# Optimization experiments

Measured on AMD Instinct MI355X. Metric: run time of the kernel, lower is better.

## Reference

```python
import jax, jax.numpy as jnp
from jax import lax
import numpy as np

B, T, D_IN, H, D_L1_IN = 128, 2048, 5, 128, 256


def _gru_layer(x, w_ih, w_hh, b_ih, b_hh, reverse):
    # x: [B,T,D]; w_ih: [3H,D]; w_hh: [3H,H]. PyTorch gate order: r, z, n.
    gx = jnp.einsum('btd,gd->btg', x, w_ih) + b_ih  # [B,T,3H] input projections, batched
    if reverse:
        gx = gx[:, ::-1]
    gx_t = jnp.swapaxes(gx, 0, 1)  # [T,B,3H]
    h0 = jnp.zeros((x.shape[0], H), x.dtype)

    def step(h, gxt):
        gh = h @ w_hh.T + b_hh  # [B,3H]
        r = jax.nn.sigmoid(gxt[:, :H] + gh[:, :H])
        z = jax.nn.sigmoid(gxt[:, H:2 * H] + gh[:, H:2 * H])
        n = jnp.tanh(gxt[:, 2 * H:] + r * gh[:, 2 * H:])
        h_new = (1.0 - z) * n + z * h
        return h_new, h_new

    _, ys = lax.scan(step, h0, gx_t)  # ys: [T,B,H]
    ys = jnp.swapaxes(ys, 0, 1)  # [B,T,H]
    if reverse:
        ys = ys[:, ::-1]
    return ys


def setup_inputs() -> dict:
    key = jax.random.key(0)
    ks = jax.random.split(key, 16)
    s0 = 1.0 / np.sqrt(H)

    def w(k, shape):
        return jax.random.uniform(k, shape, jnp.float32, -s0, s0)

    inp = {'seq': jax.random.normal(ks[0], (B, T, D_IN), jnp.float32)}
    # layer 0 forward / backward (input dim 5)
    inp['w_ih_l0f'] = w(ks[1], (3 * H, D_IN)); inp['w_hh_l0f'] = w(ks[2], (3 * H, H))
    inp['b_ih_l0f'] = w(ks[3], (3 * H,));      inp['b_hh_l0f'] = w(ks[4], (3 * H,))
    inp['w_ih_l0b'] = w(ks[5], (3 * H, D_IN)); inp['w_hh_l0b'] = w(ks[6], (3 * H, H))
    inp['b_ih_l0b'] = w(ks[7], (3 * H,));      inp['b_hh_l0b'] = w(ks[8], (3 * H,))
    # layer 1 forward / backward (input dim 256 = 2*H)
    inp['w_ih_l1f'] = w(ks[9], (3 * H, D_L1_IN));  inp['w_hh_l1f'] = w(ks[10], (3 * H, H))
    inp['b_ih_l1f'] = w(ks[11], (3 * H,));         inp['b_hh_l1f'] = w(ks[12], (3 * H,))
    inp['w_ih_l1b'] = w(ks[13], (3 * H, D_L1_IN)); inp['w_hh_l1b'] = w(ks[14], (3 * H, H))
    inp['b_ih_l1b'] = w(ks[15], (3 * H,));         inp['b_hh_l1b'] = w(ks[15], (3 * H,)) * 0.9
    # linear head
    kf = jax.random.split(ks[0], 2)
    inp['fc_w'] = w(kf[0], (1, 2 * H))
    inp['fc_b'] = w(kf[1], (1,))
    return inp


def reference(seq, w_ih_l0f, w_hh_l0f, b_ih_l0f, b_hh_l0f,
              w_ih_l0b, w_hh_l0b, b_ih_l0b, b_hh_l0b,
              w_ih_l1f, w_hh_l1f, b_ih_l1f, b_hh_l1f,
              w_ih_l1b, w_hh_l1b, b_ih_l1b, b_hh_l1b,
              fc_w, fc_b):
    # layer 0: bidirectional, concat directions
    y0f = _gru_layer(seq, w_ih_l0f, w_hh_l0f, b_ih_l0f, b_hh_l0f, reverse=False)
    y0b = _gru_layer(seq, w_ih_l0b, w_hh_l0b, b_ih_l0b, b_hh_l0b, reverse=True)
    y0 = jnp.concatenate([y0f, y0b], axis=-1)  # [B,T,256]
    # layer 1
    y1f = _gru_layer(y0, w_ih_l1f, w_hh_l1f, b_ih_l1f, b_hh_l1f, reverse=False)
    y1b = _gru_layer(y0, w_ih_l1b, w_hh_l1b, b_ih_l1b, b_hh_l1b, reverse=True)
    y1 = jnp.concatenate([y1f, y1b], axis=-1)  # [B,T,256]
    # head on last timestep
    return y1[:, -1, :] @ fc_w.T + fc_b  # [B,1]
```

## Files before the change

### kernel.cpp

```cpp
#include <hip/hip_runtime.h>
#include <hip/hip_fp16.h>
#include <cstdint>

#define B_   128
#define T_   2048
#define DIN  5
#define H_   128
#define G3   384
#define D1   256
#define CH   256
#define NCH  (T_ / CH)

typedef _Float16 half8 __attribute__((ext_vector_type(8)));
typedef float f32x4 __attribute__((ext_vector_type(4)));

__device__ __forceinline__ float sigmoid_f(float x) {
    return __builtin_amdgcn_rcpf(1.0f + __expf(-x));
}
__device__ __forceinline__ float tanh_f(float x) {
    return 1.0f - 2.0f * __builtin_amdgcn_rcpf(__expf(2.0f * x) + 1.0f);
}
__device__ __forceinline__ unsigned long long pack4h(const float* h) {
    union { __half2 h2[2]; unsigned long long u; } pk;
    pk.h2[0] = __floats2half2_rn(h[0], h[1]);
    pk.h2[1] = __floats2half2_rn(h[2], h[3]);
    return pk.u;
}
__device__ __forceinline__ f32x4 h4_to_f(unsigned long long u) {
    union { unsigned long long u; __half2 h2[2]; } p; p.u = u;
    const float2 a = __half22float2(p.h2[0]);
    const float2 b = __half22float2(p.h2[1]);
    f32x4 r; r[0] = a.x; r[1] = a.y; r[2] = b.x; r[3] = b.y; return r;
}
__device__ __forceinline__ void fast_barrier() {
    asm volatile("s_waitcnt lgkmcnt(0)\n\ts_barrier" ::: "memory");
}

__global__ __launch_bounds__(256, 1) void scan0_mfma3(
    const float* __restrict__ seq,
    const float* __restrict__ wihf, const float* __restrict__ whhf,
    const float* __restrict__ bihf, const float* __restrict__ bhhf,
    const float* __restrict__ wihb, const float* __restrict__ whhb,
    const float* __restrict__ bihb, const float* __restrict__ bhhb,
    __half* __restrict__ y0)
{
    const int tid = threadIdx.x;
    const int w  = tid >> 6;
    const int l  = tid & 63;
    const int lo = l & 15;
    const int g  = l >> 4;
    const int dir = blockIdx.x >> 3;
    const int bg  = blockIdx.x & 7;

    const float* w_ih = dir ? wihb : wihf;
    const float* w_hh = dir ? whhb : whhf;
    const float* b_ih = dir ? bihb : bihf;
    const float* b_hh = dir ? bhhb : bhhf;

    __shared__ __align__(16) char smem[2 * 16 * 512];

    half8 a_r[2][5], a_z[2][5], a_n[2][5], a_x[2];
#pragma unroll
    for (int i = 0; i < 2; ++i) {
        const int grow = (2 * w + i) * 16 + lo;
#pragma unroll
        for (int c = 0; c < 5; ++c) {
            half8 vr, vz, vn;
#pragma unroll
            for (int j = 0; j < 8; ++j) {
                const int k = c * 32 + g * 8 + j;
                float fr, fz, fn;
                if (k < 128) {
                    fr = w_hh[grow * H_ + k];
                    fz = w_hh[(128 + grow) * H_ + k];
                    fn = w_hh[(256 + grow) * H_ + k];
                } else if (k < 133) {
                    fr = w_ih[grow * DIN + (k - 128)];
                    fz = w_ih[(128 + grow) * DIN + (k - 128)];
                    fn = 0.f;
                } else if (k == 133) {
                    fr = b_ih[grow] + b_hh[grow];
                    fz = b_ih[128 + grow] + b_hh[128 + grow];
                    fn = b_hh[256 + grow];
                } else { fr = 0.f; fz = 0.f; fn = 0.f; }
                vr[j] = (_Float16)fr; vz[j] = (_Float16)fz; vn[j] = (_Float16)fn;
            }
            a_r[i][c] = vr; a_z[i][c] = vz; a_n[i][c] = vn;
        }
        half8 vx;
#pragma unroll
        for (int j = 0; j < 8; ++j) {
            const int k = 128 + g * 8 + j;
            float f = 0.f;
            if (k < 133)       f = w_ih[(256 + grow) * DIN + (k - 128)];
            else if (k == 133) f = b_ih[256 + grow];
            vx[j] = (_Float16)f;
        }
        a_x[i] = vx;
    }

#pragma unroll
    for (int q = 0; q < 4; ++q) {
        f32x4 z = {0.f, 0.f, 0.f, 0.f};
        *reinterpret_cast<f32x4*>(smem + tid * 64 + q * 16) = z;
    }
    __syncthreads();
    if (tid < 32) {
        const int row = tid & 15, bu = tid >> 4;
        *(_Float16*)(smem + bu * 8192 + row * 512 + (266 ^ ((row & 7) << 4))) =
            (_Float16)1.0f;
    }
    const bool stager = tid < 80;
    const int sb = tid / 5, sd = tid % 5;
    const size_t seqbase = (size_t)(bg * 16 + sb) * T_ * DIN + sd;
    float x_t1 = 0.f;
    if (stager) {
        const int tt0 = dir ? (T_ - 1) : 0;
        const float x0 = seq[seqbase + (size_t)tt0 * DIN];
        *(_Float16*)(smem + sb * 512 + ((256 + 2 * sd) ^ ((sb & 7) << 4))) =
            (_Float16)x0;
        const int tt1 = dir ? (T_ - 2) : 1;
        x_t1 = seq[seqbase + (size_t)tt1 * DIN];
    }
    __syncthreads();

    float h_old[2][4];
#pragma unroll
    for (int i = 0; i < 2; ++i)
#pragma unroll
        for (int q = 0; q < 4; ++q) h_old[i][q] = 0.f;

    for (int t = 0; t < T_; ++t) {
        char* cur = smem + (t & 1) * 8192;
        char* nxt = smem + ((t + 1) & 1) * 8192;

        if (stager)
            *(_Float16*)(nxt + sb * 512 + ((256 + 2 * sd) ^ ((sb & 7) << 4))) =
                (_Float16)x_t1;

        half8 bf[5];
#pragma unroll
        for (int c = 0; c < 5; ++c)
            bf[c] = *reinterpret_cast<const half8*>(
                cur + lo * 512 + ((c * 64 + g * 16) ^ ((lo & 7) << 4)));

        float x_t2 = 0.f;
        if (stager) {
            const int t2 = (t + 2 < T_) ? t + 2 : T_ - 1;
            const int tt2 = dir ? (T_ - 1 - t2) : t2;
            x_t2 = seq[seqbase + (size_t)tt2 * DIN];
        }

        f32x4 accr[2], accz[2], accn[2], accx[2];
#pragma unroll
        for (int i = 0; i < 2; ++i) {
            f32x4 zr = {0.f, 0.f, 0.f, 0.f};
            accr[i] = zr; accz[i] = zr; accn[i] = zr;
#pragma unroll
            for (int c = 0; c < 5; ++c) {
                accr[i] = __builtin_amdgcn_mfma_f32_16x16x32_f16(a_r[i][c], bf[c], accr[i], 0, 0, 0);
                accz[i] = __builtin_amdgcn_mfma_f32_16x16x32_f16(a_z[i][c], bf[c], accz[i], 0, 0, 0);
                accn[i] = __builtin_amdgcn_mfma_f32_16x16x32_f16(a_n[i][c], bf[c], accn[i], 0, 0, 0);
            }
            accx[i] = __builtin_amdgcn_mfma_f32_16x16x32_f16(a_x[i], bf[4], zr, 0, 0, 0);
        }

        const int tt = dir ? (T_ - 1 - t) : t;
#pragma unroll
        for (int i = 0; i < 2; ++i) {
            float hn[4];
#pragma unroll
            for (int q = 0; q < 4; ++q) {
                const float r = sigmoid_f(accr[i][q]);
                const float z = sigmoid_f(accz[i][q]);
                const float n = tanh_f(accx[i][q] + r * accn[i][q]);
                hn[q] = n + z * (h_old[i][q] - n);
                h_old[i][q] = hn[q];
            }
            const int j0 = (2 * w + i) * 16 + g * 4;
            const unsigned long long pu = pack4h(hn);
            *reinterpret_cast<unsigned long long*>(
                &y0[((size_t)(bg * 16 + lo) * T_ + tt) * D1 + dir * H_ + j0]) = pu;
            *reinterpret_cast<unsigned long long*>(
                nxt + lo * 512 + ((2 * j0) ^ ((lo & 7) << 4))) = pu;
        }
        x_t1 = x_t2;
        fast_barrier();
    }
}

__global__ __launch_bounds__(256, 2) void gemm1_f16(
    const __half* __restrict__ A,
    const float* __restrict__ W,
    const float* __restrict__ bias,
    __half* __restrict__ C,
    int c0)
{
    __shared__ __align__(16) _Float16 As[128][32];
    __shared__ __align__(16) _Float16 Bs[64][32];
    const int tid = threadIdx.x;
    const int wave = tid >> 6, l = tid & 63;
    const int wm = wave >> 1, wn = wave & 1;
    const int lo = l & 15, g = l >> 4;
    const int m0 = blockIdx.x * 128, n0 = blockIdx.y * 64;

    f32x4 acc[4][2];
#pragma unroll
    for (int mt = 0; mt < 4; ++mt)
#pragma unroll
        for (int nt = 0; nt < 2; ++nt) {
            f32x4 z = {0.f, 0.f, 0.f, 0.f};
            acc[mt][nt] = z;
        }

    for (int kc = 0; kc < 256; kc += 32) {
#pragma unroll
        for (int r2 = 0; r2 < 2; ++r2) {
            const int idx = tid + r2 * 256;
            const int row = idx >> 2, seg = idx & 3;
            const int m = m0 + row, bb = m >> 8, tlq = m & (CH - 1);
            const __half* src = A + ((size_t)bb * T_ + c0 + tlq) * D1 + kc + seg * 8;
            *reinterpret_cast<uint4*>(&As[row][seg * 8]) =
                *reinterpret_cast<const uint4*>(src);
        }
        {
            const int row = tid >> 2, seg = tid & 3;
            const float* srcw = W + (size_t)(n0 + row) * D1 + kc + seg * 8;
            const float4 u0 = *reinterpret_cast<const float4*>(srcw);
            const float4 u1 = *reinterpret_cast<const float4*>(srcw + 4);
            half8 hv;
            hv[0] = (_Float16)u0.x; hv[1] = (_Float16)u0.y;
            hv[2] = (_Float16)u0.z; hv[3] = (_Float16)u0.w;
            hv[4] = (_Float16)u1.x; hv[5] = (_Float16)u1.y;
            hv[6] = (_Float16)u1.z; hv[7] = (_Float16)u1.w;
            *reinterpret_cast<half8*>(&Bs[row][seg * 8]) = hv;
        }
        __syncthreads();
        half8 af[4], bfr[2];
#pragma unroll
        for (int mt = 0; mt < 4; ++mt)
            af[mt] = *reinterpret_cast<half8*>(&As[wm * 64 + mt * 16 + lo][g * 8]);
#pragma unroll
        for (int nt = 0; nt < 2; ++nt)
            bfr[nt] = *reinterpret_cast<half8*>(&Bs[wn * 32 + nt * 16 + lo][g * 8]);
#pragma unroll
        for (int mt = 0; mt < 4; ++mt)
#pragma unroll
            for (int nt = 0; nt < 2; ++nt)
                acc[mt][nt] = __builtin_amdgcn_mfma_f32_16x16x32_f16(
                    af[mt], bfr[nt], acc[mt][nt], 0, 0, 0);
        __syncthreads();
    }
#pragma unroll
    for (int nt = 0; nt < 2; ++nt) {
        const int n = n0 + wn * 32 + nt * 16 + lo;
        const float bv = bias[n];
#pragma unroll
        for (int mt = 0; mt < 4; ++mt) {
            const int mrow = m0 + wm * 64 + mt * 16 + g * 4;
#pragma unroll
            for (int q = 0; q < 4; ++q)
                C[(size_t)(mrow + q) * G3 + n] = __float2half(acc[mt][nt][q] + bv);
        }
    }
}

__global__ __launch_bounds__(256, 1) void scan1_mfma3(
    const __half* __restrict__ gxc,
    const float* __restrict__ whh, const float* __restrict__ bhh,
    float* __restrict__ h1, int c)
{
    const int tid = threadIdx.x;
    const int w = tid >> 6, l = tid & 63;
    const int lo = l & 15, g = l >> 4;
    const int grp = blockIdx.x;

    __shared__ __align__(16) char smem[2 * 16 * 256];

    half8 a_r[2][4], a_z[2][4], a_n[2][4];
    float br[2][4], bz[2][4], bn[2][4];
#pragma unroll
    for (int i = 0; i < 2; ++i) {
        const int grow = (2 * w + i) * 16 + lo;
#pragma unroll
        for (int cc = 0; cc < 4; ++cc) {
            half8 vr, vz, vn;
#pragma unroll
            for (int j = 0; j < 8; ++j) {
                const int k = cc * 32 + g * 8 + j;
                vr[j] = (_Float16)whh[grow * H_ + k];
                vz[j] = (_Float16)whh[(128 + grow) * H_ + k];
                vn[j] = (_Float16)whh[(256 + grow) * H_ + k];
            }
            a_r[i][cc] = vr; a_z[i][cc] = vz; a_n[i][cc] = vn;
        }
#pragma unroll
        for (int q = 0; q < 4; ++q) {
            const int gq = (2 * w + i) * 16 + g * 4 + q;
            br[i][q] = bhh[gq];
            bz[i][q] = bhh[128 + gq];
            bn[i][q] = bhh[256 + gq];
        }
    }

#pragma unroll
    for (int q = 0; q < 2; ++q) {
        f32x4 z = {0.f, 0.f, 0.f, 0.f};
        *reinterpret_cast<f32x4*>(smem + tid * 32 + q * 16) = z;
    }
    __syncthreads();

    float h_old[2][4];
    if (c == 0) {
#pragma unroll
        for (int i = 0; i < 2; ++i)
#pragma unroll
            for (int q = 0; q < 4; ++q) h_old[i][q] = 0.f;
    } else {
#pragma unroll
        for (int i = 0; i < 2; ++i) {
            const int j0 = (2 * w + i) * 16 + g * 4;
            const f32x4 hv = *reinterpret_cast<const f32x4*>(
                &h1[(grp * 16 + lo) * H_ + j0]);
            float hn[4];
#pragma unroll
            for (int q = 0; q < 4; ++q) { h_old[i][q] = hv[q]; hn[q] = hv[q]; }
            *reinterpret_cast<unsigned long long*>(
                smem + lo * 256 + ((2 * j0) ^ ((lo & 7) << 4))) = pack4h(hn);
        }
    }
    __syncthreads();

    const __half* gxl = gxc + (size_t)(grp * 16 + lo) * CH * G3;
    unsigned long long gxc_cur[6], gxc_nxt[6];
#pragma unroll
    for (int i = 0; i < 2; ++i) {
        const int gr0 = (2 * w + i) * 16 + g * 4;
        gxc_cur[i]     = *reinterpret_cast<const unsigned long long*>(gxl + gr0);
        gxc_cur[2 + i] = *reinterpret_cast<const unsigned long long*>(gxl + 128 + gr0);
        gxc_cur[4 + i] = *reinterpret_cast<const unsigned long long*>(gxl + 256 + gr0);
    }

    for (int t = 0; t < CH; ++t) {
        char* curb = smem + (t & 1) * 4096;
        char* nxtb = smem + ((t + 1) & 1) * 4096;

        half8 bf[4];
#pragma unroll
        for (int cc = 0; cc < 4; ++cc)
            bf[cc] = *reinterpret_cast<const half8*>(
                curb + lo * 256 + ((cc * 64 + g * 16) ^ ((lo & 7) << 4)));

        const int tn = (t + 1 < CH) ? t + 1 : t;
        const __half* p = gxl + (size_t)tn * G3;
#pragma unroll
        for (int i = 0; i < 2; ++i) {
            const int gr0 = (2 * w + i) * 16 + g * 4;
            gxc_nxt[i]     = *reinterpret_cast<const unsigned long long*>(p + gr0);
            gxc_nxt[2 + i] = *reinterpret_cast<const unsigned long long*>(p + 128 + gr0);
            gxc_nxt[4 + i] = *reinterpret_cast<const unsigned long long*>(p + 256 + gr0);
        }

        f32x4 accr[2], accz[2], accn[2];
#pragma unroll
        for (int i = 0; i < 2; ++i) {
            f32x4 zr = {0.f, 0.f, 0.f, 0.f};
            accr[i] = zr; accz[i] = zr; accn[i] = zr;
#pragma unroll
            for (int cc = 0; cc < 4; ++cc) {
                accr[i] = __builtin_amdgcn_mfma_f32_16x16x32_f16(a_r[i][cc], bf[cc], accr[i], 0, 0, 0);
                accz[i] = __builtin_amdgcn_mfma_f32_16x16x32_f16(a_z[i][cc], bf[cc], accz[i], 0, 0, 0);
                accn[i] = __builtin_amdgcn_mfma_f32_16x16x32_f16(a_n[i][cc], bf[cc], accn[i], 0, 0, 0);
            }
        }

#pragma unroll
        for (int i = 0; i < 2; ++i) {
            const f32x4 gr = h4_to_f(gxc_cur[i]);
            const f32x4 gz = h4_to_f(gxc_cur[2 + i]);
            const f32x4 gn = h4_to_f(gxc_cur[4 + i]);
            float hn[4];
#pragma unroll
            for (int q = 0; q < 4; ++q) {
                const float r = sigmoid_f(accr[i][q] + br[i][q] + gr[q]);
                const float z = sigmoid_f(accz[i][q] + bz[i][q] + gz[q]);
                const float n = tanh_f(gn[q] + r * (accn[i][q] + bn[i][q]));
                hn[q] = n + z * (h_old[i][q] - n);
                h_old[i][q] = hn[q];
            }
            const int j0 = (2 * w + i) * 16 + g * 4;
            *reinterpret_cast<unsigned long long*>(
                nxtb + lo * 256 + ((2 * j0) ^ ((lo & 7) << 4))) = pack4h(hn);
        }
#pragma unroll
        for (int i = 0; i < 6; ++i) gxc_cur[i] = gxc_nxt[i];
        fast_barrier();
    }

#pragma unroll
    for (int i = 0; i < 2; ++i) {
        const int j0 = (2 * w + i) * 16 + g * 4;
        f32x4 hv;
#pragma unroll
        for (int q = 0; q < 4; ++q) hv[q] = h_old[i][q];
        *reinterpret_cast<f32x4*>(&h1[(grp * 16 + lo) * H_ + j0]) = hv;
    }
}

__global__ __launch_bounds__(384, 1) void back1_fc(
    const __half* __restrict__ y0, const float* __restrict__ h1,
    const float* __restrict__ w_ih_1b, const float* __restrict__ b_ih_1b,
    const float* __restrict__ b_hh_1b,
    const float* __restrict__ fc_w, const float* __restrict__ fc_b,
    float* __restrict__ out)
{
    const int g = threadIdx.x;
    const int b = blockIdx.x;
    __shared__ float ylast[D1];
    __shared__ float pre_rz[2 * H_];
    __shared__ float gxn[H_], ghn[H_];
    __shared__ float hb[H_];
    __shared__ float red[H_];

    if (g < D1) ylast[g] = __half2float(y0[((size_t)b * T_ + (T_ - 1)) * D1 + g]);
    __syncthreads();

    float accb = b_ih_1b[g];
    const float* wrow = w_ih_1b + (size_t)g * D1;
#pragma unroll 8
    for (int k = 0; k < D1; k += 4) {
        const float4 v = *reinterpret_cast<const float4*>(&ylast[k]);
        const float4 wv = *reinterpret_cast<const float4*>(&wrow[k]);
        accb += v.x * wv.x + v.y * wv.y + v.z * wv.z + v.w * wv.w;
    }
    const float bh2 = b_hh_1b[g];
    if (g < 2 * H_) pre_rz[g] = accb + bh2;
    else            { gxn[g - 2 * H_] = accb; ghn[g - 2 * H_] = bh2; }
    __syncthreads();
    if (g < H_) {
        const float r = sigmoid_f(pre_rz[g]);
        const float z = sigmoid_f(pre_rz[g + H_]);
        const float n = tanh_f(gxn[g] + r * ghn[g]);
        hb[g] = (1.0f - z) * n;
    }
    __syncthreads();
    if (g < H_) red[g] = h1[b * H_ + g] * fc_w[g] + hb[g] * fc_w[H_ + g];
    __syncthreads();
    if (g == 0) {
        float s = fc_b[0];
#pragma unroll 8
        for (int k = 0; k < H_; ++k) s += red[k];
        out[b] = s;
    }
}

extern "C" void kernel_launch(void* const* d_in, const int* in_sizes, int n_in,
                              void* d_out, int out_size, void* d_ws, size_t ws_size,
                              hipStream_t stream)
{
    const float* seq      = (const float*)d_in[0];
    const float* w_ih_l0f = (const float*)d_in[1];
    const float* w_hh_l0f = (const float*)d_in[2];
    const float* b_ih_l0f = (const float*)d_in[3];
    const float* b_hh_l0f = (const float*)d_in[4];
    const float* w_ih_l0b = (const float*)d_in[5];
    const float* w_hh_l0b = (const float*)d_in[6];
    const float* b_ih_l0b = (const float*)d_in[7];
    const float* b_hh_l0b = (const float*)d_in[8];
    const float* w_ih_l1f = (const float*)d_in[9];
    const float* w_hh_l1f = (const float*)d_in[10];
    const float* b_ih_l1f = (const float*)d_in[11];
    const float* b_hh_l1f = (const float*)d_in[12];
    const float* w_ih_l1b = (const float*)d_in[13];
    const float* b_ih_l1b = (const float*)d_in[15];
    const float* b_hh_l1b = (const float*)d_in[16];
    const float* fc_w     = (const float*)d_in[17];
    const float* fc_b     = (const float*)d_in[18];
    float* out = (float*)d_out;

    __half* y0h = (__half*)d_ws;
    __half* gxc = (__half*)((char*)d_ws +
                  (size_t)B_ * T_ * D1 * sizeof(__half));
    float*  h1  = (float*)(gxc + (size_t)B_ * CH * G3);

    hipLaunchKernelGGL(scan0_mfma3, dim3(16), dim3(256), 0, stream,
        seq, w_ih_l0f, w_hh_l0f, b_ih_l0f, b_hh_l0f,
             w_ih_l0b, w_hh_l0b, b_ih_l0b, b_hh_l0b, y0h);

    for (int ci = 0; ci < NCH; ++ci) {
        hipLaunchKernelGGL(gemm1_f16, dim3(B_ * CH / 128, 6), dim3(256), 0, stream,
            y0h, w_ih_l1f, b_ih_l1f, gxc, ci * CH);
        hipLaunchKernelGGL(scan1_mfma3, dim3(8), dim3(256), 0, stream,
            gxc, w_hh_l1f, b_hh_l1f, h1, ci);
    }

    hipLaunchKernelGGL(back1_fc, dim3(B_), dim3(384), 0, stream,
        y0h, h1, w_ih_l1b, b_ih_l1b, b_hh_l1b, fc_w, fc_b, out);
}
```

Baseline: 3.666 ms.

## Overlap layer-1 input GEMM with recurrent scan and widen layer-0 scan

Layer 1 now uses a single fused kernel per chunk: 8 blocks run the recurrent scan on chunk i-1 while 768 blocks compute the input-projection GEMM for chunk i into a double-buffered gx workspace. This hides the GEMM behind the serial scan. The chunk size is halved to 128, which shrinks each buffer but doubles the number of launches. Separately, the layer-0 scan uses 512 threads with one 16-row gate tile per wave instead of two, cutting per-step MFMA and activation work per wave at the cost of more waves at each barrier.

Result: faster. 3.434 ms (-6.3%).

```diff
diff --git a/kernel.cpp b/kernel.cpp
--- a/kernel.cpp
+++ b/kernel.cpp
@@ -8,8 +8,9 @@
 #define H_   128
 #define G3   384
 #define D1   256
-#define CH   256
+#define CH   128
 #define NCH  (T_ / CH)
+#define LOG2CH 7
 
 typedef _Float16 half8 __attribute__((ext_vector_type(8)));
 typedef float f32x4 __attribute__((ext_vector_type(4)));
@@ -36,7 +37,7 @@
     asm volatile("s_waitcnt lgkmcnt(0)\n\ts_barrier" ::: "memory");
 }
 
-__global__ __launch_bounds__(256, 1) void scan0_mfma3(
+__global__ __launch_bounds__(512, 2) void scan0_mfma4(
     const float* __restrict__ seq,
     const float* __restrict__ wihf, const float* __restrict__ whhf,
     const float* __restrict__ bihf, const float* __restrict__ bhhf,
@@ -59,10 +60,9 @@
 
     __shared__ __align__(16) char smem[2 * 16 * 512];
 
-    half8 a_r[2][5], a_z[2][5], a_n[2][5], a_x[2];
-#pragma unroll
-    for (int i = 0; i < 2; ++i) {
-        const int grow = (2 * w + i) * 16 + lo;
+    half8 a_r[5], a_z[5], a_n[5], a_x;
+    {
+        const int grow = w * 16 + lo;
 #pragma unroll
         for (int c = 0; c < 5; ++c) {
             half8 vr, vz, vn;
@@ -85,7 +85,7 @@
                 } else { fr = 0.f; fz = 0.f; fn = 0.f; }
                 vr[j] = (_Float16)fr; vz[j] = (_Float16)fz; vn[j] = (_Float16)fn;
             }
-            a_r[i][c] = vr; a_z[i][c] = vz; a_n[i][c] = vn;
+            a_r[c] = vr; a_z[c] = vz; a_n[c] = vn;
         }
         half8 vx;
 #pragma unroll
@@ -96,13 +96,13 @@
             else if (k == 133) f = b_ih[256 + grow];
             vx[j] = (_Float16)f;
         }
-        a_x[i] = vx;
-    }
-
-#pragma unroll
-    for (int q = 0; q < 4; ++q) {
+        a_x = vx;
+    }
+
+#pragma unroll
+    for (int q = 0; q < 2; ++q) {
         f32x4 z = {0.f, 0.f, 0.f, 0.f};
-        *reinterpret_cast<f32x4*>(smem + tid * 64 + q * 16) = z;
+        *reinterpret_cast<f32x4*>(smem + tid * 32 + q * 16) = z;
     }
     __syncthreads();
     if (tid < 32) {
@@ -124,11 +124,9 @@
     }
     __syncthreads();
 
-    float h_old[2][4];
-#pragma unroll
-    for (int i = 0; i < 2; ++i)
-#pragma unroll
-        for (int q = 0; q < 4; ++q) h_old[i][q] = 0.f;
+    float h_old[4];
+#pragma unroll
+    for (int q = 0; q < 4; ++q) h_old[q] = 0.f;
 
     for (int t = 0; t < T_; ++t) {
         char* cur = smem + (t & 1) * 8192;
@@ -151,33 +149,28 @@
             x_t2 = seq[seqbase + (size_t)tt2 * DIN];
         }
 
-        f32x4 accr[2], accz[2], accn[2], accx[2];
-#pragma unroll
-        for (int i = 0; i < 2; ++i) {
-            f32x4 zr = {0.f, 0.f, 0.f, 0.f};
-            accr[i] = zr; accz[i] = zr; accn[i] = zr;
-#pragma unroll
-            for (int c = 0; c < 5; ++c) {
-                accr[i] = __builtin_amdgcn_mfma_f32_16x16x32_f16(a_r[i][c], bf[c], accr[i], 0, 0, 0);
-                accz[i] = __builtin_amdgcn_mfma_f32_16x16x32_f16(a_z[i][c], bf[c], accz[i], 0, 0, 0);
-                accn[i] = __builtin_amdgcn_mfma_f32_16x16x32_f16(a_n[i][c], bf[c], accn[i], 0, 0, 0);
+        f32x4 zr = {0.f, 0.f, 0.f, 0.f};
+        f32x4 accr = zr, accz = zr, accn = zr, accx;
+#pragma unroll
+        for (int c = 0; c < 5; ++c) {
+            accr = __builtin_amdgcn_mfma_f32_16x16x32_f16(a_r[c], bf[c], accr, 0, 0, 0);
+            accz = __builtin_amdgcn_mfma_f32_16x16x32_f16(a_z[c], bf[c], accz, 0, 0, 0);
+            accn = __builtin_amdgcn_mfma_f32_16x16x32_f16(a_n[c], bf[c], accn, 0, 0, 0);
+        }
+        accx = __builtin_amdgcn_mfma_f32_16x16x32_f16(a_x, bf[4], zr, 0, 0, 0);
+
+        const int tt = dir ? (T_ - 1 - t) : t;
+        {
+            float hn[4];
+#pragma unroll
+            for (int q = 0; q < 4; ++q) {
+                const float r = sigmoid_f(accr[q]);
+                const float z = sigmoid_f(accz[q]);
+                const float n = tanh_f(accx[q] + r * accn[q]);
+                hn[q] = n + z * (h_old[q] - n);
+                h_old[q] = hn[q];
             }
-            accx[i] = __builtin_amdgcn_mfma_f32_16x16x32_f16(a_x[i], bf[4], zr, 0, 0, 0);
-        }
-
-        const int tt = dir ? (T_ - 1 - t) : t;
-#pragma unroll
-        for (int i = 0; i < 2; ++i) {
-            float hn[4];
-#pragma unroll
-            for (int q = 0; q < 4; ++q) {
-                const float r = sigmoid_f(accr[i][q]);
-                const float z = sigmoid_f(accz[i][q]);
-                const float n = tanh_f(accx[i][q] + r * accn[i][q]);
-                hn[q] = n + z * (h_old[i][q] - n);
-                h_old[i][q] = hn[q];
-            }
-            const int j0 = (2 * w + i) * 16 + g * 4;
+            const int j0 = w * 16 + g * 4;
             const unsigned long long pu = pack4h(hn);
             *reinterpret_cast<unsigned long long*>(
                 &y0[((size_t)(bg * 16 + lo) * T_ + tt) * D1 + dir * H_ + j0]) = pu;
@@ -189,20 +182,159 @@
     }
 }
 
-__global__ __launch_bounds__(256, 2) void gemm1_f16(
-    const __half* __restrict__ A,
-    const float* __restrict__ W,
-    const float* __restrict__ bias,
-    __half* __restrict__ C,
-    int c0)
+__device__ __forceinline__ void scan1_role(
+    char* smem,
+    const __half* __restrict__ gxc,
+    const float* __restrict__ whh, const float* __restrict__ bhh,
+    float* __restrict__ h1, int c)
 {
-    __shared__ __align__(16) _Float16 As[128][32];
-    __shared__ __align__(16) _Float16 Bs[64][32];
+    const int tid = threadIdx.x;
+    const int w = tid >> 6, l = tid & 63;
+    const int lo = l & 15, g = l >> 4;
+    const int grp = blockIdx.x;
+
+    half8 a_r[2][4], a_z[2][4], a_n[2][4];
+    float br[2][4], bz[2][4], bn[2][4];
+#pragma unroll
+    for (int i = 0; i < 2; ++i) {
+        const int grow = (2 * w + i) * 16 + lo;
+#pragma unroll
+        for (int cc = 0; cc < 4; ++cc) {
+            half8 vr, vz, vn;
+#pragma unroll
+            for (int j = 0; j < 8; ++j) {
+                const int k = cc * 32 + g * 8 + j;
+                vr[j] = (_Float16)whh[grow * H_ + k];
+                vz[j] = (_Float16)whh[(128 + grow) * H_ + k];
+                vn[j] = (_Float16)whh[(256 + grow) * H_ + k];
+            }
+            a_r[i][cc] = vr; a_z[i][cc] = vz; a_n[i][cc] = vn;
+        }
+#pragma unroll
+        for (int q = 0; q < 4; ++q) {
+            const int gq = (2 * w + i) * 16 + g * 4 + q;
+            br[i][q] = bhh[gq];
+            bz[i][q] = bhh[128 + gq];
+            bn[i][q] = bhh[256 + gq];
+        }
+    }
+
+#pragma unroll
+    for (int q = 0; q < 2; ++q) {
+        f32x4 z = {0.f, 0.f, 0.f, 0.f};
+        *reinterpret_cast<f32x4*>(smem + tid * 32 + q * 16) = z;
+    }
+    __syncthreads();
+
+    float h_old[2][4];
+    if (c == 0) {
+#pragma unroll
+        for (int i = 0; i < 2; ++i)
+#pragma unroll
+            for (int q = 0; q < 4; ++q) h_old[i][q] = 0.f;
+    } else {
+#pragma unroll
+        for (int i = 0; i < 2; ++i) {
+            const int j0 = (2 * w + i) * 16 + g * 4;
+            const f32x4 hv = *reinterpret_cast<const f32x4*>(
+                &h1[(grp * 16 + lo) * H_ + j0]);
+            float hn[4];
+#pragma unroll
+            for (int q = 0; q < 4; ++q) { h_old[i][q] = hv[q]; hn[q] = hv[q]; }
+            *reinterpret_cast<unsigned long long*>(
+                smem + lo * 256 + ((2 * j0) ^ ((lo & 7) << 4))) = pack4h(hn);
+        }
+    }
+    __syncthreads();
+
+    const __half* gxl = gxc + (size_t)(grp * 16 + lo) * CH * G3;
+    unsigned long long gxc_cur[6], gxc_nxt[6];
+#pragma unroll
+    for (int i = 0; i < 2; ++i) {
+        const int gr0 = (2 * w + i) * 16 + g * 4;
+        gxc_cur[i]     = *reinterpret_cast<const unsigned long long*>(gxl + gr0);
+        gxc_cur[2 + i] = *reinterpret_cast<const unsigned long long*>(gxl + 128 + gr0);
+        gxc_cur[4 + i] = *reinterpret_cast<const unsigned long long*>(gxl + 256 + gr0);
+    }
+
+    for (int t = 0; t < CH; ++t) {
+        char* curb = smem + (t & 1) * 4096;
+        char* nxtb = smem + ((t + 1) & 1) * 4096;
+
+        half8 bf[4];
+#pragma unroll
+        for (int cc = 0; cc < 4; ++cc)
+            bf[cc] = *reinterpret_cast<const half8*>(
+                curb + lo * 256 + ((cc * 64 + g * 16) ^ ((lo & 7) << 4)));
+
+        const int tn = (t + 1 < CH) ? t + 1 : t;
+        const __half* p = gxl + (size_t)tn * G3;
+#pragma unroll
+        for (int i = 0; i < 2; ++i) {
+            const int gr0 = (2 * w + i) * 16 + g * 4;
+            gxc_nxt[i]     = *reinterpret_cast<const unsigned long long*>(p + gr0);
+            gxc_nxt[2 + i] = *reinterpret_cast<const unsigned long long*>(p + 128 + gr0);
+            gxc_nxt[4 + i] = *reinterpret_cast<const unsigned long long*>(p + 256 + gr0);
+        }
+
+        f32x4 accr[2], accz[2], accn[2];
+#pragma unroll
+        for (int i = 0; i < 2; ++i) {
+            f32x4 zr = {0.f, 0.f, 0.f, 0.f};
+            accr[i] = zr; accz[i] = zr; accn[i] = zr;
+#pragma unroll
+            for (int cc = 0; cc < 4; ++cc) {
+                accr[i] = __builtin_amdgcn_mfma_f32_16x16x32_f16(a_r[i][cc], bf[cc], accr[i], 0, 0, 0);
+                accz[i] = __builtin_amdgcn_mfma_f32_16x16x32_f16(a_z[i][cc], bf[cc], accz[i], 0, 0, 0);
+                accn[i] = __builtin_amdgcn_mfma_f32_16x16x32_f16(a_n[i][cc], bf[cc], accn[i], 0, 0, 0);
+            }
+        }
+
+#pragma unroll
+        for (int i = 0; i < 2; ++i) {
+            const f32x4 gr = h4_to_f(gxc_cur[i]);
+            const f32x4 gz = h4_to_f(gxc_cur[2 + i]);
+            const f32x4 gn = h4_to_f(gxc_cur[4 + i]);
+            float hn[4];
+#pragma unroll
+            for (int q = 0; q < 4; ++q) {
+                const float r = sigmoid_f(accr[i][q] + br[i][q] + gr[q]);
+                const float z = sigmoid_f(accz[i][q] + bz[i][q] + gz[q]);
+                const float n = tanh_f(gn[q] + r * (accn[i][q] + bn[i][q]));
+                hn[q] = n + z * (h_old[i][q] - n);
+                h_old[i][q] = hn[q];
+            }
+            const int j0 = (2 * w + i) * 16 + g * 4;
+            *reinterpret_cast<unsigned long long*>(
+                nxtb + lo * 256 + ((2 * j0) ^ ((lo & 7) << 4))) = pack4h(hn);
+        }
+#pragma unroll
+        for (int i = 0; i < 6; ++i) gxc_cur[i] = gxc_nxt[i];
+        fast_barrier();
+    }
+
+#pragma unroll
+    for (int i = 0; i < 2; ++i) {
+        const int j0 = (2 * w + i) * 16 + g * 4;
+        f32x4 hv;
+#pragma unroll
+        for (int q = 0; q < 4; ++q) hv[q] = h_old[i][q];
+        *reinterpret_cast<f32x4*>(&h1[(grp * 16 + lo) * H_ + j0]) = hv;
+    }
+}
+
+__device__ __forceinline__ void gemm_role(
+    char* smem, int rb,
+    const __half* __restrict__ A, const float* __restrict__ W,
+    const float* __restrict__ bias, __half* __restrict__ C, int c0)
+{
+    _Float16 (*As)[32] = reinterpret_cast<_Float16(*)[32]>(smem);
+    _Float16 (*Bs)[32] = reinterpret_cast<_Float16(*)[32]>(smem + 8192);
     const int tid = threadIdx.x;
     const int wave = tid >> 6, l = tid & 63;
     const int wm = wave >> 1, wn = wave & 1;
     const int lo = l & 15, g = l >> 4;
-    const int m0 = blockIdx.x * 128, n0 = blockIdx.y * 64;
+    const int m0 = (rb & 127) * 128, n0 = (rb >> 7) * 64;
 
     f32x4 acc[4][2];
 #pragma unroll
@@ -218,7 +350,7 @@
         for (int r2 = 0; r2 < 2; ++r2) {
             const int idx = tid + r2 * 256;
             const int row = idx >> 2, seg = idx & 3;
-            const int m = m0 + row, bb = m >> 8, tlq = m & (CH - 1);
+            const int m = m0 + row, bb = m >> LOG2CH, tlq = m & (CH - 1);
             const __half* src = A + ((size_t)bb * T_ + c0 + tlq) * D1 + kc + seg * 8;
             *reinterpret_cast<uint4*>(&As[row][seg * 8]) =
                 *reinterpret_cast<const uint4*>(src);
@@ -265,145 +397,24 @@
     }
 }
 
-__global__ __launch_bounds__(256, 1) void scan1_mfma3(
-    const __half* __restrict__ gxc,
+__global__ __launch_bounds__(256, 1) void fused_l1(
+    const __half* __restrict__ y0,
+    const float* __restrict__ W1f, const float* __restrict__ b1f,
+    __half* __restrict__ gbufA, __half* __restrict__ gbufB,
     const float* __restrict__ whh, const float* __restrict__ bhh,
-    float* __restrict__ h1, int c)
+    float* __restrict__ h1, int ci_scan, int ci_gemm)
 {
-    const int tid = threadIdx.x;
-    const int w = tid >> 6, l = tid & 63;
-    const int lo = l & 15, g = l >> 4;
-    const int grp = blockIdx.x;
-
-    __shared__ __align__(16) char smem[2 * 16 * 256];
-
-    half8 a_r[2][4], a_z[2][4], a_n[2][4];
-    float br[2][4], bz[2][4], bn[2][4];
-#pragma unroll
-    for (int i = 0; i < 2; ++i) {
-        const int grow = (2 * w + i) * 16 + lo;
-#pragma unroll
-        for (int cc = 0; cc < 4; ++cc) {
-            half8 vr, vz, vn;
-#pragma unroll
-            for (int j = 0; j < 8; ++j) {
-                const int k = cc * 32 + g * 8 + j;
-                vr[j] = (_Float16)whh[grow * H_ + k];
-                vz[j] = (_Float16)whh[(128 + grow) * H_ + k];
-                vn[j] = (_Float16)whh[(256 + grow) * H_ + k];
-            }
-            a_r[i][cc] = vr; a_z[i][cc] = vz; a_n[i][cc] = vn;
-        }
-#pragma unroll
-        for (int q = 0; q < 4; ++q) {
-            const int gq = (2 * w + i) * 16 + g * 4 + q;
-            br[i][q] = bhh[gq];
-            bz[i][q] = bhh[128 + gq];
-            bn[i][q] = bhh[256 + gq];
-        }
-    }
-
-#pragma unroll
-    for (int q = 0; q < 2; ++q) {
-        f32x4 z = {0.f, 0.f, 0.f, 0.f};
-        *reinterpret_cast<f32x4*>(smem + tid * 32 + q * 16) = z;
-    }
-    __syncthreads();
-
-    float h_old[2][4];
-    if (c == 0) {
-#pragma unroll
-        for (int i = 0; i < 2; ++i)
-#pragma unroll
-            for (int q = 0; q < 4; ++q) h_old[i][q] = 0.f;
+    __shared__ __align__(16) char smem[12288];
+    if (blockIdx.x < 8) {
+        if (ci_scan >= 0) {
+            const __half* gxc = (ci_scan & 1) ? gbufB : gbufA;
+            scan1_role(smem, gxc, whh, bhh, h1, ci_scan);
+        }
     } else {
-#pragma unroll
-        for (int i = 0; i < 2; ++i) {
-            const int j0 = (2 * w + i) * 16 + g * 4;
-            const f32x4 hv = *reinterpret_cast<const f32x4*>(
-                &h1[(grp * 16 + lo) * H_ + j0]);
-            float hn[4];
-#pragma unroll
-            for (int q = 0; q < 4; ++q) { h_old[i][q] = hv[q]; hn[q] = hv[q]; }
-            *reinterpret_cast<unsigned long long*>(
-                smem + lo * 256 + ((2 * j0) ^ ((lo & 7) << 4))) = pack4h(hn);
-        }
-    }
-    __syncthreads();
-
-    const __half* gxl = gxc + (size_t)(grp * 16 + lo) * CH * G3;
-    unsigned long long gxc_cur[6], gxc_nxt[6];
-#pragma unroll
-    for (int i = 0; i < 2; ++i) {
-        const int gr0 = (2 * w + i) * 16 + g * 4;
-        gxc_cur[i]     = *reinterpret_cast<const unsigned long long*>(gxl + gr0);
-        gxc_cur[2 + i] = *reinterpret_cast<const unsigned long long*>(gxl + 128 + gr0);
-        gxc_cur[4 + i] = *reinterpret_cast<const unsigned long long*>(gxl + 256 + gr0);
-    }
-
-    for (int t = 0; t < CH; ++t) {
-        char* curb = smem + (t & 1) * 4096;
-        char* nxtb = smem + ((t + 1) & 1) * 4096;
-
-        half8 bf[4];
-#pragma unroll
-        for (int cc = 0; cc < 4; ++cc)
-            bf[cc] = *reinterpret_cast<const half8*>(
-                curb + lo * 256 + ((cc * 64 + g * 16) ^ ((lo & 7) << 4)));
-
-        const int tn = (t + 1 < CH) ? t + 1 : t;
-        const __half* p = gxl + (size_t)tn * G3;
-#pragma unroll
-        for (int i = 0; i < 2; ++i) {
-            const int gr0 = (2 * w + i) * 16 + g * 4;
-            gxc_nxt[i]     = *reinterpret_cast<const unsigned long long*>(p + gr0);
-            gxc_nxt[2 + i] = *reinterpret_cast<const unsigned long long*>(p + 128 + gr0);
-            gxc_nxt[4 + i] = *reinterpret_cast<const unsigned long long*>(p + 256 + gr0);
-        }
-
-        f32x4 accr[2], accz[2], accn[2];
-#pragma unroll
-        for (int i = 0; i < 2; ++i) {
-            f32x4 zr = {0.f, 0.f, 0.f, 0.f};
-            accr[i] = zr; accz[i] = zr; accn[i] = zr;
-#pragma unroll
-            for (int cc = 0; cc < 4; ++cc) {
-                accr[i] = __builtin_amdgcn_mfma_f32_16x16x32_f16(a_r[i][cc], bf[cc], accr[i], 0, 0, 0);
-                accz[i] = __builtin_amdgcn_mfma_f32_16x16x32_f16(a_z[i][cc], bf[cc], accz[i], 0, 0, 0);
-                accn[i] = __builtin_amdgcn_mfma_f32_16x16x32_f16(a_n[i][cc], bf[cc], accn[i], 0, 0, 0);
-            }
-        }
-
-#pragma unroll
-        for (int i = 0; i < 2; ++i) {
-            const f32x4 gr = h4_to_f(gxc_cur[i]);
-            const f32x4 gz = h4_to_f(gxc_cur[2 + i]);
-            const f32x4 gn = h4_to_f(gxc_cur[4 + i]);
-            float hn[4];
-#pragma unroll
-            for (int q = 0; q < 4; ++q) {
-                const float r = sigmoid_f(accr[i][q] + br[i][q] + gr[q]);
-                const float z = sigmoid_f(accz[i][q] + bz[i][q] + gz[q]);
-                const float n = tanh_f(gn[q] + r * (accn[i][q] + bn[i][q]));
-                hn[q] = n + z * (h_old[i][q] - n);
-                h_old[i][q] = hn[q];
-            }
-            const int j0 = (2 * w + i) * 16 + g * 4;
-            *reinterpret_cast<unsigned long long*>(
-                nxtb + lo * 256 + ((2 * j0) ^ ((lo & 7) << 4))) = pack4h(hn);
-        }
-#pragma unroll
-        for (int i = 0; i < 6; ++i) gxc_cur[i] = gxc_nxt[i];
-        fast_barrier();
-    }
-
-#pragma unroll
-    for (int i = 0; i < 2; ++i) {
-        const int j0 = (2 * w + i) * 16 + g * 4;
-        f32x4 hv;
-#pragma unroll
-        for (int q = 0; q < 4; ++q) hv[q] = h_old[i][q];
-        *reinterpret_cast<f32x4*>(&h1[(grp * 16 + lo) * H_ + j0]) = hv;
+        if (ci_gemm < NCH) {
+            __half* gxc = (ci_gemm & 1) ? gbufB : gbufA;
+            gemm_role(smem, (int)blockIdx.x - 8, y0, W1f, b1f, gxc, ci_gemm * CH);
+        }
     }
 }
 
@@ -478,20 +489,21 @@
     const float* fc_b     = (const float*)d_in[18];
     float* out = (float*)d_out;
 
-    __half* y0h = (__half*)d_ws;
-    __half* gxc = (__half*)((char*)d_ws +
-                  (size_t)B_ * T_ * D1 * sizeof(__half));
-    float*  h1  = (float*)(gxc + (size_t)B_ * CH * G3);
-
-    hipLaunchKernelGGL(scan0_mfma3, dim3(16), dim3(256), 0, stream,
+    const size_t y0_bytes = (size_t)B_ * T_ * D1 * sizeof(__half);
+    const size_t gx_bytes = (size_t)B_ * CH * G3 * sizeof(__half);
+    __half* y0h   = (__half*)d_ws;
+    __half* gbufA = (__half*)((char*)d_ws + y0_bytes);
+    __half* gbufB = (__half*)((char*)d_ws + y0_bytes + gx_bytes);
+    float*  h1    = (float*)((char*)d_ws + y0_bytes + 2 * gx_bytes);
+
+    hipLaunchKernelGGL(scan0_mfma4, dim3(16), dim3(512), 0, stream,
         seq, w_ih_l0f, w_hh_l0f, b_ih_l0f, b_hh_l0f,
              w_ih_l0b, w_hh_l0b, b_ih_l0b, b_hh_l0b, y0h);
 
-    for (int ci = 0; ci < NCH; ++ci) {
-        hipLaunchKernelGGL(gemm1_f16, dim3(B_ * CH / 128, 6), dim3(256), 0, stream,
-            y0h, w_ih_l1f, b_ih_l1f, gxc, ci * CH);
-        hipLaunchKernelGGL(scan1_mfma3, dim3(8), dim3(256), 0, stream,
-            gxc, w_hh_l1f, b_hh_l1f, h1, ci);
+    for (int i = 0; i <= NCH; ++i) {
+        hipLaunchKernelGGL(fused_l1, dim3(8 + 768), dim3(256), 0, stream,
+            y0h, w_ih_l1f, b_ih_l1f, gbufA, gbufB,
+            w_hh_l1f, b_hh_l1f, h1, i - 1, i);
     }
 
     hipLaunchKernelGGL(back1_fc, dim3(B_), dim3(384), 0, stream,
```
